# Performance work log

Measured on AMD Instinct MI355X. Metric: run time of the kernel, lower is better.

The kernel has to match this reference:

```python
import jax, jax.numpy as jnp
from jax import lax
import numpy as np

B, C_IN, H, W = 16, 3, 256, 256
D = 256          # d_model
K = 512          # codebook_size
COMMIT_W = 1.0
BN_EPS = 1e-5


def setup_inputs() -> dict:
    key = jax.random.key(0)
    ks = jax.random.split(key, 3)
    x = jax.random.normal(ks[0], (B, C_IN, H, W), dtype=jnp.float32)
    conv_w = jax.random.normal(ks[1], (D, C_IN, 3, 3), dtype=jnp.float32) * 0.1
    conv_b = jnp.zeros((D,), dtype=jnp.float32)
    bn_gamma = jnp.ones((D,), dtype=jnp.float32)
    bn_beta = jnp.zeros((D,), dtype=jnp.float32)
    bn_mean = jnp.zeros((D,), dtype=jnp.float32)
    bn_var = jnp.ones((D,), dtype=jnp.float32)
    codebook = jax.random.normal(ks[2], (K, D), dtype=jnp.float32)
    return {"x": x, "conv_w": conv_w, "conv_b": conv_b,
            "bn_gamma": bn_gamma, "bn_beta": bn_beta,
            "bn_mean": bn_mean, "bn_var": bn_var, "codebook": codebook}


def _encode(x, conv_w, conv_b, bn_gamma, bn_beta, bn_mean, bn_var):
    # Conv2d(3, D, k=3, s=1, p=1)
    y = lax.conv_general_dilated(x, conv_w, window_strides=(1, 1),
                                 padding=[(1, 1), (1, 1)],
                                 dimension_numbers=("NCHW", "OIHW", "NCHW"))
    y = y + conv_b[None, :, None, None]
    # MaxPool2d(2, 2)
    y = lax.reduce_window(y, -jnp.inf, lax.max, (1, 1, 2, 2), (1, 1, 2, 2), "VALID")
    # BatchNorm2d (inference, running stats)
    inv = bn_gamma * lax.rsqrt(bn_var + BN_EPS)
    y = (y - bn_mean[None, :, None, None]) * inv[None, :, None, None] \
        + bn_beta[None, :, None, None]
    # exact GELU (torch default)
    return jax.nn.gelu(y, approximate=False)


def _vq(fmap, codebook):
    b, d, h, w = fmap.shape
    xe = fmap.transpose(0, 2, 3, 1).reshape(b, h * w, d)        # [B, N, D]
    # squared euclidean distances to codebook: [B, N, K]
    x2 = jnp.sum(xe * xe, axis=-1, keepdims=True)
    c2 = jnp.sum(codebook * codebook, axis=-1)
    dist = x2 - 2.0 * jnp.einsum("bnd,kd->bnk", xe, codebook) + c2[None, None, :]
    idx = jnp.argmin(dist, axis=-1)                              # [B, N] int
    quant = codebook[idx]                                        # [B, N, D]
    commit_loss = COMMIT_W * jnp.mean((lax.stop_gradient(quant) - xe) ** 2)
    # straight-through
    quant_st = xe + lax.stop_gradient(quant - xe)
    quant_fmap = quant_st.reshape(b, h, w, d).transpose(0, 3, 1, 2)
    return quant_fmap, idx.reshape(b, h, w), commit_loss


def reference(x, conv_w, conv_b, bn_gamma, bn_beta, bn_mean, bn_var, codebook):
    fmap = _encode(x, conv_w, conv_b, bn_gamma, bn_beta, bn_mean, bn_var)
    quant, indices, commit_loss = _vq(fmap, codebook)
    return quant, indices, commit_loss
```

## Files before the change

kernel.cpp:

```cpp
#include <hip/hip_runtime.h>
#include <math.h>

#define CIN 3
#define HIN 256
#define WIN 256
#define ND 256
#define NK 512
#define HP 128
#define WP 128
#define NPOS (HP*WP)
#define NB 16
#define QOUT ((size_t)NB*(size_t)ND*(size_t)NPOS)
#define IDXOUT ((size_t)NB*(size_t)NPOS)
#define LOSS_OFF (QOUT + IDXOUT)
#define REFINE_EPS 0.09f
#define MAX_REFINE 16
#define BN_EPSF 1e-5f
#define SSHIFT 256.0f

#define HR 6
#define HC 66
#define HCH 70
#define HALO_N (CIN*HR*HC)

typedef _Float16 f16x8 __attribute__((ext_vector_type(8)));
typedef float    f32x4 __attribute__((ext_vector_type(4)));

#define WS_VQH_B 2048
#define WS_CWH_B 264192
#define WS_SC_B  280576
#define WS_SH_B  281600

struct SMem {
    alignas(16) unsigned short xe[64 * ND];
    float halo[HALO_N];
    _Float16 halo_h[CIN * HR * HCH];
    unsigned int ms1[4 * 64];
    unsigned int ms2[4 * 64];
    unsigned int ms3[4 * 64];
    int   bestidx[64];
    int   refine_pos[MAX_REFINE];
    int   refine_c[MAX_REFINE][3];
    int   refine_count;
    float sqbuf[4];
    float s1tot;
    double red[32];
};

__device__ __forceinline__ unsigned pack_pos(float s, int n) {
    return (__builtin_bit_cast(unsigned, s) & 0xFFFFFE00u) | (unsigned)n;
}
__device__ __forceinline__ float unpack_pos(unsigned u) {
    return __builtin_bit_cast(float, u & 0xFFFFFE00u);
}
__device__ __forceinline__ void insert3(unsigned u, unsigned& b1,
                                        unsigned& b2, unsigned& b3) {
    unsigned t1 = min(u, b1), h1 = max(u, b1);
    b1 = t1;
    unsigned t2 = min(h1, b2), h2 = max(h1, b2);
    b2 = t2;
    b3 = min(h2, b3);
}

__global__ void prep_kernel(const float* __restrict__ cb,
                            const float* __restrict__ conv_w,
                            const float* __restrict__ conv_b,
                            const float* __restrict__ gamma,
                            const float* __restrict__ beta,
                            const float* __restrict__ mean,
                            const float* __restrict__ var,
                            float* __restrict__ c2s,
                            _Float16* __restrict__ vqh,
                            _Float16* __restrict__ cwh,
                            float* __restrict__ scale,
                            float* __restrict__ shift,
                            float* __restrict__ loss_out) {
    const int blk = blockIdx.x;
    const int t = threadIdx.x;
    if (blk < 64) {
        const int fr = blk * 4 + (t >> 6);
        const int lane = t & 63;
        const int nt = fr >> 3, s = fr & 7;
        const int n = nt * 16 + (lane & 15);
        const int dbase = s * 32 + ((lane >> 4) << 3);
        const float* src = cb + (size_t)n * ND + dbase;
        f16x8 vh;
        #pragma unroll
        for (int e = 0; e < 8; e++) vh[e] = (_Float16)src[e];
        *reinterpret_cast<f16x8*>(&vqh[(size_t)fr * 512 + lane * 8]) = vh;
    } else if (blk == 64) {
        for (int c = t; c < NK; c += 256) {
            const float4* row = reinterpret_cast<const float4*>(cb + (size_t)c * ND);
            float s = 0.f;
            #pragma unroll 8
            for (int i = 0; i < ND / 4; i++) {
                float4 v = row[i];
                s = fmaf(v.x, v.x, s); s = fmaf(v.y, v.y, s);
                s = fmaf(v.z, v.z, s); s = fmaf(v.w, v.w, s);
            }
            c2s[c] = 0.5f * s + SSHIFT;
        }
        {
            int ch = t;
            float inv = gamma[ch] / sqrtf(var[ch] + BN_EPSF);
            scale[ch] = inv;
            shift[ch] = (conv_b[ch] - mean[ch]) * inv + beta[ch];
        }
        if (t == 0) *loss_out = 0.f;
    } else {
        const int lane = t & 63;
        for (int fr = t >> 6; fr < 16; fr += 4) {
            const int n = fr * 16 + (lane & 15);
            f16x8 vh;
            #pragma unroll
            for (int e = 0; e < 8; e++) {
                int k = ((lane >> 4) << 3) + e;
                vh[e] = (k < 27) ? (_Float16)conv_w[n * 27 + k] : (_Float16)0.f;
            }
            *reinterpret_cast<f16x8*>(&cwh[(size_t)fr * 512 + lane * 8]) = vh;
        }
    }
}

__global__ __launch_bounds__(256, 2)
void vqvae_kernel(const float* __restrict__ x, const float* __restrict__ conv_w,
                  const float* __restrict__ cb, const float* __restrict__ c2s,
                  const float* __restrict__ conv_bp,
                  const float* __restrict__ gamma, const float* __restrict__ beta,
                  const float* __restrict__ mean, const float* __restrict__ var,
                  const _Float16* __restrict__ vqh,
                  const _Float16* __restrict__ cwh,
                  const float* __restrict__ scale,
                  const float* __restrict__ shift,
                  float* __restrict__ out) {
    __shared__ SMem sm;
    const int t = threadIdx.x;
    const int l = t & 63;
    const int wv = t >> 6;
    const int blk = blockIdx.x;
    const int b = blk >> 8;
    const int tile = blk & 255;
    const int ty0 = (tile >> 2) * 2;
    const int tx0 = (tile & 3) * 32;

    {
        const int iy0 = ty0 * 2 - 1;
        const int ix0 = tx0 * 2 - 1;
        for (int e = t; e < HALO_N; e += 256) {
            int c = e / (HR * HC);
            int rem = e - c * (HR * HC);
            int r = rem / HC;
            int cc = rem - r * HC;
            int iy = iy0 + r, ix = ix0 + cc;
            float v = 0.f;
            if (iy >= 0 && iy < HIN && ix >= 0 && ix < WIN)
                v = x[(((size_t)b * CIN + c) * HIN + iy) * WIN + ix];
            sm.halo[e] = v;
            sm.halo_h[c * (HR * HCH) + r * HCH + cc] = (_Float16)v;
        }
        if (t == 0) sm.refine_count = 0;
    }

    int hoff2[8];
    #pragma unroll
    for (int e = 0; e < 8; e++) {
        int k = ((l >> 4) << 3) + e;
        int c = k / 9;
        int r9 = k - c * 9;
        int dy = r9 / 3;
        int dx = r9 - dy * 3;
        hoff2[e] = (k < 27) ? (c * (HR * HCH) + dy * HCH + dx) : 0;
    }

    float sc4[4], sh4[4];
    #pragma unroll
    for (int j = 0; j < 4; j++) {
        int ch = wv * 64 + j * 16 + (l & 15);
        sc4[j] = scale[ch];
        sh4[j] = shift[ch];
    }
    __syncthreads();

    float sq = 0.f;
    #pragma unroll 1
    for (int mc = 0; mc < 4; mc++) {
        f16x8 ah[4];
        #pragma unroll
        for (int i = 0; i < 4; i++) {
            const int m16 = l & 15;
            const int p = i * 4 + (m16 >> 2);
            const int q = m16 & 3;
            const int pos = mc * 16 + p;
            const int py = pos >> 5, px = pos & 31;
            const int cy = py * 2 + (q >> 1), cx = px * 2 + (q & 1);
            const int base = cy * HCH + cx;
            #pragma unroll
            for (int e = 0; e < 8; e++)
                ah[i][e] = sm.halo_h[base + hoff2[e]];
        }
        #pragma unroll 1
        for (int jh = 0; jh < 2; jh++) {
            f16x8 bw0 = *reinterpret_cast<const f16x8*>(
                &cwh[(wv * 4 + jh * 2 + 0) * 512 + l * 8]);
            f16x8 bw1 = *reinterpret_cast<const f16x8*>(
                &cwh[(wv * 4 + jh * 2 + 1) * 512 + l * 8]);
            f32x4 acc[4][2];
            #pragma unroll
            for (int i = 0; i < 4; i++) {
                acc[i][0] = (f32x4){0.f, 0.f, 0.f, 0.f};
                acc[i][1] = (f32x4){0.f, 0.f, 0.f, 0.f};
            }
            #pragma unroll
            for (int i = 0; i < 4; i++) {
                acc[i][0] = __builtin_amdgcn_mfma_f32_16x16x32_f16(ah[i], bw0, acc[i][0], 0, 0, 0);
                acc[i][1] = __builtin_amdgcn_mfma_f32_16x16x32_f16(ah[i], bw1, acc[i][1], 0, 0, 0);
            }
            #pragma unroll
            for (int i = 0; i < 4; i++) {
                const int pos = mc * 16 + i * 4 + (l >> 4);
                #pragma unroll
                for (int jj = 0; jj < 2; jj++) {
                    const int j = jh * 2 + jj;
                    f32x4 a4 = acc[i][jj];
                    float m = fmaxf(fmaxf(a4[0], a4[1]), fmaxf(a4[2], a4[3]));
                    float bn = fmaf(m, sc4[j], sh4[j]);
                    float g = 0.5f * bn * (1.0f + erff(bn * 0.7071067811865475f));
                    sq = fmaf(g, g, sq);
                    _Float16 h = (_Float16)g;
                    int ch = wv * 64 + j * 16 + (l & 15);
                    int slot = pos * ND + (((ch >> 3) ^ (pos & 7)) << 3) + (ch & 7);
                    sm.xe[slot] = __builtin_bit_cast(unsigned short, h);
                }
            }
        }
    }
    #pragma unroll
    for (int off = 32; off; off >>= 1) sq += __shfl_xor(sq, off, 64);
    if (l == 0) sm.sqbuf[wv] = sq;
    __syncthreads();

    unsigned pb1[4], pb2[4], pb3[4];
    #pragma unroll
    for (int j = 0; j < 4; j++) {
        pb1[j] = 0xFFFFFFFFu; pb2[j] = 0xFFFFFFFFu; pb3[j] = 0xFFFFFFFFu;
    }

    #pragma unroll 1
    for (int cg = 0; cg < 4; ++cg) {
        f32x4 acc[2][4];
        #pragma unroll
        for (int tt = 0; tt < 2; tt++)
            #pragma unroll
            for (int j = 0; j < 4; j++) acc[tt][j] = (f32x4){0.f, 0.f, 0.f, 0.f};

        #pragma unroll 2
        for (int s = 0; s < 8; ++s) {
            f16x8 bx[4];
            #pragma unroll
            for (int j = 0; j < 4; ++j) {
                int n = j * 16 + (l & 15);
                int g = s * 4 + (l >> 4);
                int gp = g ^ (n & 7);
                bx[j] = *reinterpret_cast<const f16x8*>(&sm.xe[n * ND + gp * 8]);
            }
            #pragma unroll
            for (int tt = 0; tt < 2; ++tt) {
                int ct = wv * 8 + cg * 2 + tt;
                f16x8 ac = *reinterpret_cast<const f16x8*>(
                    &vqh[(size_t)(ct * 8 + s) * 512 + l * 8]);
                #pragma unroll
                for (int j = 0; j < 4; ++j)
                    acc[tt][j] = __builtin_amdgcn_mfma_f32_16x16x32_f16(ac, bx[j], acc[tt][j], 0, 0, 0);
            }
        }
        #pragma unroll
        for (int tt = 0; tt < 2; ++tt) {
            int cbase = (wv * 8 + cg * 2 + tt) * 16 + ((l >> 4) << 2);
            float4 c2q = *reinterpret_cast<const float4*>(&c2s[cbase]);
            #pragma unroll
            for (int j = 0; j < 4; ++j) {
                insert3(pack_pos(c2q.x - acc[tt][j][0], cbase + 0), pb1[j], pb2[j], pb3[j]);
                insert3(pack_pos(c2q.y - acc[tt][j][1], cbase + 1), pb1[j], pb2[j], pb3[j]);
                insert3(pack_pos(c2q.z - acc[tt][j][2], cbase + 2), pb1[j], pb2[j], pb3[j]);
                insert3(pack_pos(c2q.w - acc[tt][j][3], cbase + 3), pb1[j], pb2[j], pb3[j]);
            }
        }
    }

    #pragma unroll
    for (int j = 0; j < 4; ++j) {
        unsigned a1 = pb1[j], a2 = pb2[j], a3 = pb3[j];
        #pragma unroll
        for (int off = 16; off <= 32; off <<= 1) {
            unsigned o1 = __shfl_xor((int)a1, off, 64);
            unsigned o2 = __shfl_xor((int)a2, off, 64);
            unsigned o3 = __shfl_xor((int)a3, off, 64);
            insert3(o1, a1, a2, a3);
            insert3(o2, a1, a2, a3);
            insert3(o3, a1, a2, a3);
        }
        if (l < 16) {
            sm.ms1[wv * 64 + j * 16 + l] = a1;
            sm.ms2[wv * 64 + j * 16 + l] = a2;
            sm.ms3[wv * 64 + j * 16 + l] = a3;
        }
    }
    __syncthreads();

    if (t < 64) {
        unsigned b1 = 0xFFFFFFFFu, b2 = 0xFFFFFFFFu, b3 = 0xFFFFFFFFu;
        #pragma unroll
        for (int w = 0; w < 4; ++w) {
            insert3(sm.ms1[w * 64 + t], b1, b2, b3);
            insert3(sm.ms2[w * 64 + t], b1, b2, b3);
            insert3(sm.ms3[w * 64 + t], b1, b2, b3);
        }
        sm.bestidx[t] = (int)(b1 & 511u);
        float s1f = unpack_pos(b1), s2f = unpack_pos(b2);
        if (s2f - s1f < REFINE_EPS) {
            int slot = atomicAdd(&sm.refine_count, 1);
            if (slot < MAX_REFINE) {
                sm.refine_pos[slot] = t;
                sm.refine_c[slot][0] = (int)(b1 & 511u);
                sm.refine_c[slot][1] = (int)(b2 & 511u);
                sm.refine_c[slot][2] = (int)(b3 & 511u);
            }
        }
        float s1 = s1f;
        #pragma unroll
        for (int off = 32; off; off >>= 1) s1 += __shfl_xor(s1, off, 64);
        if (t == 0) sm.s1tot = s1;
    }
    __syncthreads();

    {
        int nref = sm.refine_count;
        if (nref > MAX_REFINE) nref = MAX_REFINE;
        for (int rr = 0; rr < nref; rr++) {
            const int pos = sm.refine_pos[rr];
            const int d = t;
            const int py = pos >> 5, px = pos & 31;
            const int r0 = py * 2, c0 = px * 2;
            double s00, s01, s10, s11;
            s00 = s01 = s10 = s11 = (double)conv_bp[d];
            for (int c = 0; c < 3; c++) {
                for (int r = 0; r < 4; r++) {
                    const float* hrow = &sm.halo[c * (HR * HC) + (r0 + r) * HC + c0];
                    double v0 = (double)hrow[0];
                    double v1 = (double)hrow[1];
                    double v2 = (double)hrow[2];
                    double v3 = (double)hrow[3];
                    if (r <= 2) {
                        double w0 = (double)conv_w[d*27 + c*9 + r*3 + 0];
                        double w1 = (double)conv_w[d*27 + c*9 + r*3 + 1];
                        double w2 = (double)conv_w[d*27 + c*9 + r*3 + 2];
                        s00 = fma(w0, v0, s00); s00 = fma(w1, v1, s00); s00 = fma(w2, v2, s00);
                        s01 = fma(w0, v1, s01); s01 = fma(w1, v2, s01); s01 = fma(w2, v3, s01);
                    }
                    if (r >= 1) {
                        double w0 = (double)conv_w[d*27 + c*9 + (r-1)*3 + 0];
                        double w1 = (double)conv_w[d*27 + c*9 + (r-1)*3 + 1];
                        double w2 = (double)conv_w[d*27 + c*9 + (r-1)*3 + 2];
                        s10 = fma(w0, v0, s10); s10 = fma(w1, v1, s10); s10 = fma(w2, v2, s10);
                        s11 = fma(w0, v1, s11); s11 = fma(w1, v2, s11); s11 = fma(w2, v3, s11);
                    }
                }
            }
            double m = fmax(fmax(s00, s01), fmax(s10, s11));
            double bn = (m - (double)mean[d]) * ((double)gamma[d] /
                        sqrt((double)var[d] + 1e-5)) + (double)beta[d];
            double xd = 0.5 * bn * (1.0 + erf(bn * 0.70710678118654752440));
            double p[3], q[3];
            #pragma unroll
            for (int k = 0; k < 3; k++) {
                double cv = (double)cb[(size_t)sm.refine_c[rr][k] * ND + d];
                p[k] = xd * cv;
                q[k] = cv * cv;
            }
            #pragma unroll
            for (int k = 0; k < 3; k++) {
                for (int off = 32; off; off >>= 1) {
                    p[k] += __shfl_xor(p[k], off, 64);
                    q[k] += __shfl_xor(q[k], off, 64);
                }
            }
            if ((t & 63) == 0) {
                #pragma unroll
                for (int k = 0; k < 3; k++) {
                    sm.red[wv * 8 + k * 2 + 0] = p[k];
                    sm.red[wv * 8 + k * 2 + 1] = q[k];
                }
            }
            __syncthreads();
            if (t == 0) {
                double bsc = 1e300; int bidx = 0x7fffffff;
                #pragma unroll
                for (int k = 0; k < 3; k++) {
                    double dot = sm.red[k*2] + sm.red[8 + k*2] + sm.red[16 + k*2] + sm.red[24 + k*2];
                    double cs  = sm.red[k*2+1] + sm.red[8 + k*2+1] + sm.red[16 + k*2+1] + sm.red[24 + k*2+1];
                    double sc = 0.5 * cs - dot;
                    int ci = sm.refine_c[rr][k];
                    if (sc < bsc || (sc == bsc && ci < bidx)) { bsc = sc; bidx = ci; }
                }
                sm.bestidx[pos] = bidx;
            }
            __syncthreads();
        }
    }
    __syncthreads();

    if (t < 64) {
        const int hw = (ty0 + (t >> 5)) * WP + tx0 + (t & 31);
        out[QOUT + (size_t)b * NPOS + hw] = (float)sm.bestidx[t];
    }
    {
        const int code = sm.bestidx[l];
        const int hw = (ty0 + (l >> 5)) * WP + tx0 + (l & 31);
        const float* crow = cb + (size_t)code * ND + wv * 64;
        float* qb = out + (size_t)b * ND * NPOS + hw;
        #pragma unroll
        for (int k4 = 0; k4 < 16; ++k4) {
            float4 cv = *reinterpret_cast<const float4*>(&crow[k4 * 4]);
            const size_t d0 = (size_t)(wv * 64 + k4 * 4);
            qb[(d0 + 0) * NPOS] = cv.x;
            qb[(d0 + 1) * NPOS] = cv.y;
            qb[(d0 + 2) * NPOS] = cv.z;
            qb[(d0 + 3) * NPOS] = cv.w;
        }
    }
    if (t == 0) {
        float tot = sm.sqbuf[0] + sm.sqbuf[1] + sm.sqbuf[2] + sm.sqbuf[3]
                  + 2.0f * (sm.s1tot - 64.0f * SSHIFT);
        atomicAdd(out + LOSS_OFF, tot * (1.0f / 67108864.0f));
    }
}

extern "C" void kernel_launch(void* const* d_in, const int* in_sizes, int n_in,
                              void* d_out, int out_size, void* d_ws, size_t ws_size,
                              hipStream_t stream) {
    const float* x      = (const float*)d_in[0];
    const float* conv_w = (const float*)d_in[1];
    const float* conv_b = (const float*)d_in[2];
    const float* gammap = (const float*)d_in[3];
    const float* betap  = (const float*)d_in[4];
    const float* meanp  = (const float*)d_in[5];
    const float* varp   = (const float*)d_in[6];
    const float* cb     = (const float*)d_in[7];
    float* out = (float*)d_out;

    char* wsb = (char*)d_ws;
    float*    c2w  = (float*)wsb;
    _Float16* vqh  = (_Float16*)(wsb + WS_VQH_B);
    _Float16* cwh  = (_Float16*)(wsb + WS_CWH_B);
    float*    scp  = (float*)(wsb + WS_SC_B);
    float*    shp  = (float*)(wsb + WS_SH_B);

    prep_kernel<<<66, 256, 0, stream>>>(cb, conv_w, conv_b, gammap, betap,
                                        meanp, varp, c2w, vqh, cwh, scp, shp,
                                        out + LOSS_OFF);
    vqvae_kernel<<<NB * 256, 256, 0, stream>>>(x, conv_w, cb, c2w, conv_b,
                                               gammap, betap, meanp, varp,
                                               vqh, cwh, scp, shp, out);
}
```

Measured before the change: 482.7 us.

## Use fast polynomial GELU, fold codebook norm into MFMA init, raise occupancy

Replaces erff in the GELU with an Abramowitz-Stegun polynomial built on a hardware reciprocal and a fast exp. It also negates the fp16 codebook copy and starts the distance accumulators at the half-norm term, which removes the per-element subtraction in the argmin epilogue. The launch bounds ask for three blocks per SM instead of two, which may force register spills. The polynomial erf carries roughly 1e-7 absolute error, which could perturb argmin near-ties, though a refine pass appears to exist.

After: 466.4 us. 3.4% less time.

```diff
diff --git a/kernel.cpp b/kernel.cpp
--- a/kernel.cpp
+++ b/kernel.cpp
@@ -60,6 +60,21 @@
     unsigned t2 = min(h1, b2), h2 = max(h1, b2);
     b2 = t2;
     b3 = min(h2, b3);
+}
+
+__device__ __forceinline__ float gelu_exact(float v) {
+    float z = v * 0.7071067811865476f;
+    float az = fabsf(z);
+    float t = __builtin_amdgcn_rcpf(fmaf(0.3275911f, az, 1.0f));
+    float p = fmaf(1.061405429f, t, -1.453152027f);
+    p = fmaf(p, t, 1.421413741f);
+    p = fmaf(p, t, -0.284496736f);
+    p = fmaf(p, t, 0.254829592f);
+    p = p * t;
+    float e = __expf(-az * az);
+    float erf_az = fmaf(-p, e, 1.0f);
+    float er = copysignf(erf_az, z);
+    return 0.5f * v * (1.0f + er);
 }
 
 __global__ void prep_kernel(const float* __restrict__ cb,
@@ -86,7 +101,7 @@
         const float* src = cb + (size_t)n * ND + dbase;
         f16x8 vh;
         #pragma unroll
-        for (int e = 0; e < 8; e++) vh[e] = (_Float16)src[e];
+        for (int e = 0; e < 8; e++) vh[e] = (_Float16)(-src[e]);
         *reinterpret_cast<f16x8*>(&vqh[(size_t)fr * 512 + lane * 8]) = vh;
     } else if (blk == 64) {
         for (int c = t; c < NK; c += 256) {
@@ -122,7 +137,7 @@
     }
 }
 
-__global__ __launch_bounds__(256, 2)
+__global__ __launch_bounds__(256, 3)
 void vqvae_kernel(const float* __restrict__ x, const float* __restrict__ conv_w,
                   const float* __restrict__ cb, const float* __restrict__ c2s,
                   const float* __restrict__ conv_bp,
@@ -224,7 +239,7 @@
                     f32x4 a4 = acc[i][jj];
                     float m = fmaxf(fmaxf(a4[0], a4[1]), fmaxf(a4[2], a4[3]));
                     float bn = fmaf(m, sc4[j], sh4[j]);
-                    float g = 0.5f * bn * (1.0f + erff(bn * 0.7071067811865475f));
+                    float g = gelu_exact(bn);
                     sq = fmaf(g, g, sq);
                     _Float16 h = (_Float16)g;
                     int ch = wv * 64 + j * 16 + (l & 15);
@@ -249,9 +264,13 @@
     for (int cg = 0; cg < 4; ++cg) {
         f32x4 acc[2][4];
         #pragma unroll
-        for (int tt = 0; tt < 2; tt++)
-            #pragma unroll
-            for (int j = 0; j < 4; j++) acc[tt][j] = (f32x4){0.f, 0.f, 0.f, 0.f};
+        for (int tt = 0; tt < 2; tt++) {
+            int cbase = (wv * 8 + cg * 2 + tt) * 16 + ((l >> 4) << 2);
+            float4 c2q = *reinterpret_cast<const float4*>(&c2s[cbase]);
+            f32x4 ci = {c2q.x, c2q.y, c2q.z, c2q.w};
+            #pragma unroll
+            for (int j = 0; j < 4; j++) acc[tt][j] = ci;
+        }
 
         #pragma unroll 2
         for (int s = 0; s < 8; ++s) {
@@ -276,13 +295,12 @@
         #pragma unroll
         for (int tt = 0; tt < 2; ++tt) {
             int cbase = (wv * 8 + cg * 2 + tt) * 16 + ((l >> 4) << 2);
-            float4 c2q = *reinterpret_cast<const float4*>(&c2s[cbase]);
             #pragma unroll
             for (int j = 0; j < 4; ++j) {
-                insert3(pack_pos(c2q.x - acc[tt][j][0], cbase + 0), pb1[j], pb2[j], pb3[j]);
-                insert3(pack_pos(c2q.y - acc[tt][j][1], cbase + 1), pb1[j], pb2[j], pb3[j]);
-                insert3(pack_pos(c2q.z - acc[tt][j][2], cbase + 2), pb1[j], pb2[j], pb3[j]);
-                insert3(pack_pos(c2q.w - acc[tt][j][3], cbase + 3), pb1[j], pb2[j], pb3[j]);
+                insert3(pack_pos(acc[tt][j][0], cbase + 0), pb1[j], pb2[j], pb3[j]);
+                insert3(pack_pos(acc[tt][j][1], cbase + 1), pb1[j], pb2[j], pb3[j]);
+                insert3(pack_pos(acc[tt][j][2], cbase + 2), pb1[j], pb2[j], pb3[j]);
+                insert3(pack_pos(acc[tt][j][3], cbase + 3), pb1[j], pb2[j], pb3[j]);
             }
         }
     }
```
